# Kernel optimization log

Hardware: AMD Instinct MI355X
Metric: run time of the kernel (lower is better)

Reference implementation:

```python
import jax, jax.numpy as jnp
import numpy as np

B, T, I, R, H = 8, 2048, 128, 1024, 256
LEAKY = 1.0           # leaky_rate
SPECTRAL_RADIUS = 0.9


def setup_inputs() -> dict:
    key = jax.random.key(0)
    ks = jax.random.split(key, 8)
    u = jax.random.normal(ks[0], (B, T, I), dtype=jnp.float32)
    # ESN cell weights (fixed random reservoir)
    w_in = jax.random.normal(ks[1], (R, I), dtype=jnp.float32) * (1.0 / np.sqrt(I))  # input_scaling=1
    w = jax.random.normal(ks[2], (R, R), dtype=jnp.float32) * (SPECTRAL_RADIUS / np.sqrt(R))
    w_bias = jnp.zeros((R,), dtype=jnp.float32)  # bias_scaling=0
    # PCA stand-in: fixed linear projection reservoir -> pca space
    w_pca = jax.random.normal(ks[3], (R, H), dtype=jnp.float32) * (1.0 / np.sqrt(R))
    # gate weights: torch.rand -> uniform [0,1)
    wzp = jax.random.uniform(ks[4], (H, H), dtype=jnp.float32)
    wzh = jax.random.uniform(ks[5], (H, H), dtype=jnp.float32)
    bz = jax.random.uniform(ks[6], (H,), dtype=jnp.float32)
    return {"u": u, "w_in": w_in, "w": w, "w_bias": w_bias,
            "w_pca": w_pca, "wzp": wzp, "wzh": wzh, "bz": bz}


def reference(u, w_in, w, w_bias, w_pca, wzp, wzh, bz):
    Bn = u.shape[0]
    Rd = w.shape[0]
    Hd = bz.shape[0]
    # Precompute input drive for all timesteps: (T, B, R)
    uin = jnp.swapaxes(jnp.einsum('bti,ri->btr', u, w_in) + w_bias, 0, 1)

    # ESN leaky reservoir recurrence: x_t = (1-a)x_{t-1} + a*tanh(W_in u_t + W x_{t-1} + b)
    def res_step(x, u_t):
        x_new = (1.0 - LEAKY) * x + LEAKY * jnp.tanh(u_t + x @ w.T)
        return x_new, x_new

    x0 = jnp.zeros((Bn, Rd), dtype=u.dtype)
    _, res_states = jax.lax.scan(res_step, x0, uin)          # (T, B, R)

    # PCA projection (linear stand-in for fitted IncrementalPCA)
    pca_states = jnp.einsum('tbr,rh->tbh', res_states, w_pca)  # (T, B, H)

    # Gated recurrence: z_t = sigmoid(Wzp p_t + Wzh h_{t-1} + bz); h_t = (1-z)*h + z*p
    def gate_step(h, p):
        z = jax.nn.sigmoid(p @ wzp.T + h @ wzh.T + bz)
        h_new = (1.0 - z) * h + z * p
        return h_new, h_new

    h0 = jnp.zeros((Bn, Hd), dtype=u.dtype)  # per-batch reset_hidden()
    _, hidden_states = jax.lax.scan(gate_step, h0, pca_states)  # (T, B, H)
    return jnp.swapaxes(hidden_states, 0, 1)                    # (B, T, H)
```

## Files before the change

### kernel.cpp

```cpp
#include <hip/hip_runtime.h>

#define TSTEPS 2048
#define NCHAIN 8
#define RDIM 1024
#define IDIM 128
#define HDIM 256
#define NB 16
#define NTHR 512
#define NBLOCKS (NB * NCHAIN)

typedef unsigned long long u64_t;

#define PIN(x) asm volatile("" : "+v"(x))

__device__ __forceinline__ u64_t aload64(const u64_t* p) {
  return __hip_atomic_load(p, __ATOMIC_RELAXED, __HIP_MEMORY_SCOPE_AGENT);
}
__device__ __forceinline__ void astore64(u64_t* p, u64_t v) {
  __hip_atomic_store(p, v, __ATOMIC_RELAXED, __HIP_MEMORY_SCOPE_AGENT);
}
__device__ __forceinline__ u64_t pack(float v, unsigned tag) {
  return ((u64_t)tag << 32) | (u64_t)__float_as_uint(v);
}
__device__ __forceinline__ float val_of(u64_t q) { return __uint_as_float((unsigned)q); }
__device__ __forceinline__ unsigned tag_of(u64_t q) { return (unsigned)(q >> 32); }

__device__ __forceinline__ float wave_sum(float v) {
  v += __shfl_xor(v, 1);
  v += __shfl_xor(v, 2);
  v += __shfl_xor(v, 4);
  v += __shfl_xor(v, 8);
  v += __shfl_xor(v, 16);
  v += __shfl_xor(v, 32);
  return v;
}

__global__ __launch_bounds__(NTHR, 1) void esn_fused(
    const float* __restrict__ u, const float* __restrict__ w_in,
    const float* __restrict__ w, const float* __restrict__ w_bias,
    const float* __restrict__ w_pca, const float* __restrict__ wzp,
    const float* __restrict__ wzh, const float* __restrict__ bz,
    float* __restrict__ out,
    u64_t* __restrict__ x_buf,
    u64_t* __restrict__ p_buf,
    u64_t* __restrict__ h_buf)
{
  const int bid = blockIdx.x;
  const int chain = bid & 7;
  const int sub = bid >> 3;
  const int tid = threadIdx.x;
  const int wave = tid >> 6;
  const int lane = tid & 63;

  __shared__ float lds_x[2][RDIM];
  __shared__ float lds_p[2][HDIM];
  __shared__ float lds_h[2][HDIM];

  const int rrow0 = sub * 64 + wave * 8;
  float4 WA[8][4];
  #pragma unroll
  for (int j = 0; j < 8; ++j)
    #pragma unroll
    for (int i = 0; i < 4; ++i)
      WA[j][i] = *reinterpret_cast<const float4*>(
          w + (size_t)(rrow0 + j) * RDIM + lane * 16 + i * 4);
  float2 Wi[8];
  #pragma unroll
  for (int j = 0; j < 8; ++j)
    Wi[j] = *reinterpret_cast<const float2*>(w_in + (size_t)(rrow0 + j) * IDIM + lane * 2);
  float wb = (lane < 8) ? w_bias[rrow0 + lane] : 0.f;

  const int pcol0 = sub * 16 + wave * 2;
  float Wp[2][16];
  #pragma unroll
  for (int j = 0; j < 2; ++j)
    #pragma unroll
    for (int k = 0; k < 16; ++k)
      Wp[j][k] = w_pca[(size_t)(lane * 16 + k) * HDIM + pcol0 + j];

  const int grow0 = sub * 16 + wave * 2;
  float4 Zp[2], Zh[2];
  #pragma unroll
  for (int j = 0; j < 2; ++j) {
    Zp[j] = *reinterpret_cast<const float4*>(wzp + (size_t)(grow0 + j) * HDIM + lane * 4);
    Zh[j] = *reinterpret_cast<const float4*>(wzh + (size_t)(grow0 + j) * HDIM + lane * 4);
  }
  float bzr = (lane < 2) ? bz[grow0 + lane] : 0.f;

  #pragma unroll
  for (int j = 0; j < 8; ++j)
    #pragma unroll
    for (int i = 0; i < 4; ++i) {
      PIN(WA[j][i].x); PIN(WA[j][i].y); PIN(WA[j][i].z); PIN(WA[j][i].w);
    }
  #pragma unroll
  for (int j = 0; j < 8; ++j) { PIN(Wi[j].x); PIN(Wi[j].y); }
  #pragma unroll
  for (int j = 0; j < 2; ++j)
    #pragma unroll
    for (int k = 0; k < 16; ++k) PIN(Wp[j][k]);
  #pragma unroll
  for (int j = 0; j < 2; ++j) {
    PIN(Zp[j].x); PIN(Zp[j].y); PIN(Zp[j].z); PIN(Zp[j].w);
    PIN(Zh[j].x); PIN(Zh[j].y); PIN(Zh[j].z); PIN(Zh[j].w);
  }
  PIN(wb); PIN(bzr);

  for (int s = 0; s < TSTEPS + 2; ++s) {
    const int cur = s & 1;

    float xc[16];
    const bool xc_valid = (s >= 1 && s <= TSTEPS);
    if (xc_valid) {
      #pragma unroll
      for (int k = 0; k < 16; ++k) xc[k] = lds_x[cur][k * 64 + lane];
    }

    if (s < TSTEPS) {
      float acc[8];
      float2 uu = *reinterpret_cast<const float2*>(
          u + ((size_t)chain * TSTEPS + s) * IDIM + lane * 2);
      #pragma unroll
      for (int j = 0; j < 8; ++j) acc[j] = Wi[j].x * uu.x + Wi[j].y * uu.y;
      if (s > 0) {
        #pragma unroll
        for (int j = 0; j < 8; ++j) {
          float a = acc[j];
          #pragma unroll
          for (int i = 0; i < 4; ++i) {
            a += WA[j][i].x * xc[i * 4 + 0];
            a += WA[j][i].y * xc[i * 4 + 1];
            a += WA[j][i].z * xc[i * 4 + 2];
            a += WA[j][i].w * xc[i * 4 + 3];
          }
          acc[j] = a;
        }
      }
      #pragma unroll
      for (int j = 0; j < 8; ++j) acc[j] = wave_sum(acc[j]);
      float v = acc[0];
      #pragma unroll
      for (int j = 1; j < 8; ++j) v = (lane == j) ? acc[j] : v;
      if (lane < 8)
        astore64(x_buf + (((s & 1) * NCHAIN) + chain) * RDIM + rrow0 + lane,
                 pack(tanhf(v + wb), (unsigned)(s + 1)));
    }

    if (xc_valid) {
      const int t = s - 1;
      float a0 = 0.f, a1 = 0.f;
      #pragma unroll
      for (int k = 0; k < 16; ++k) { a0 += Wp[0][k] * xc[k]; a1 += Wp[1][k] * xc[k]; }
      a0 = wave_sum(a0);
      a1 = wave_sum(a1);
      float v = (lane == 1) ? a1 : a0;
      if (lane < 2)
        astore64(p_buf + (((t & 3) * NCHAIN) + chain) * HDIM + pcol0 + lane,
                 pack(v, (unsigned)(t + 1)));
    }

    if (s >= 2) {
      const int t = s - 2;
      float pc[4], hc[4];
      #pragma unroll
      for (int k = 0; k < 4; ++k) pc[k] = lds_p[cur][k * 64 + lane];
      if (t > 0) {
        #pragma unroll
        for (int k = 0; k < 4; ++k) hc[k] = lds_h[cur][k * 64 + lane];
      } else {
        hc[0] = hc[1] = hc[2] = hc[3] = 0.f;
      }
      float a0 = Zp[0].x * pc[0] + Zp[0].y * pc[1] + Zp[0].z * pc[2] + Zp[0].w * pc[3]
               + Zh[0].x * hc[0] + Zh[0].y * hc[1] + Zh[0].z * hc[2] + Zh[0].w * hc[3];
      float a1 = Zp[1].x * pc[0] + Zp[1].y * pc[1] + Zp[1].z * pc[2] + Zp[1].w * pc[3]
               + Zh[1].x * hc[0] + Zh[1].y * hc[1] + Zh[1].z * hc[2] + Zh[1].w * hc[3];
      a0 = wave_sum(a0);
      a1 = wave_sum(a1);
      float v = (lane == 1) ? a1 : a0;
      if (lane < 2) {
        const int row = grow0 + lane;
        float z = 1.f / (1.f + expf(-(v + bzr)));
        float pt = lds_p[cur][(row & 3) * 64 + (row >> 2)];
        float hp = (t > 0) ? lds_h[cur][(row & 3) * 64 + (row >> 2)] : 0.f;
        float hnew = hp + z * (pt - hp);
        astore64(h_buf + (((t & 3) * NCHAIN) + chain) * HDIM + row,
                 pack(hnew, (unsigned)(t + 1)));
        out[((size_t)chain * TSTEPS + t) * HDIM + row] = hnew;
      }
    }

    const int nxt = (s + 1) & 1;
    if (wave == 0) {
      if (s <= TSTEPS - 1) {
        const u64_t* xp =
            x_buf + (((s & 1) * NCHAIN) + chain) * RDIM + lane * 16;
        const unsigned want = (unsigned)(s + 1);
        u64_t q[16];
        unsigned it = 0;
        for (;;) {
          bool ok = true;
          #pragma unroll
          for (int k = 0; k < 16; ++k) q[k] = aload64(xp + k);
          #pragma unroll
          for (int k = 0; k < 16; ++k) ok = ok & (tag_of(q[k]) == want);
          if (ok) break;
          __builtin_amdgcn_s_sleep(1);
          if (++it > (1u << 17)) break;
        }
        #pragma unroll
        for (int k = 0; k < 16; ++k) lds_x[nxt][k * 64 + lane] = val_of(q[k]);
      }
    } else if (wave == 1) {
      const bool needp = (s >= 1 && s <= TSTEPS);
      const bool needh = (s >= 2 && s <= TSTEPS);
      if (needp) {
        const u64_t* pvp =
            p_buf + ((((s - 1) & 3) * NCHAIN) + chain) * HDIM + lane * 4;
        const u64_t* hvp =
            h_buf + ((((s - 2) & 3) * NCHAIN) + chain) * HDIM + lane * 4;
        const unsigned wantp = (unsigned)s;
        const unsigned wanth = (unsigned)(s - 1);
        u64_t qp[4], qh[4];
        unsigned it = 0;
        for (;;) {
          bool ok = true;
          #pragma unroll
          for (int k = 0; k < 4; ++k) qp[k] = aload64(pvp + k);
          if (needh) {
            #pragma unroll
            for (int k = 0; k < 4; ++k) qh[k] = aload64(hvp + k);
          }
          #pragma unroll
          for (int k = 0; k < 4; ++k) ok = ok & (tag_of(qp[k]) == wantp);
          if (needh) {
            #pragma unroll
            for (int k = 0; k < 4; ++k) ok = ok & (tag_of(qh[k]) == wanth);
          }
          if (ok) break;
          __builtin_amdgcn_s_sleep(1);
          if (++it > (1u << 17)) break;
        }
        #pragma unroll
        for (int k = 0; k < 4; ++k) lds_p[nxt][k * 64 + lane] = val_of(qp[k]);
        if (needh) {
          #pragma unroll
          for (int k = 0; k < 4; ++k) lds_h[nxt][k * 64 + lane] = val_of(qh[k]);
        }
      }
    }
    __syncthreads();
  }
}

extern "C" void kernel_launch(void* const* d_in, const int* in_sizes, int n_in,
                              void* d_out, int out_size, void* d_ws, size_t ws_size,
                              hipStream_t stream) {
  const float* ptrs[8] = {nullptr};
  const int want[8] = {TSTEPS * NCHAIN * IDIM, RDIM * IDIM, RDIM * RDIM, RDIM,
                       RDIM * HDIM, HDIM * HDIM, HDIM * HDIM, HDIM};
  if (n_in == 8) {
    int used[8] = {0};
    for (int k = 0; k < 8; ++k)
      for (int i = 0; i < n_in; ++i)
        if (!used[i] && in_sizes[i] == want[k]) {
          ptrs[k] = (const float*)d_in[i]; used[i] = 1; break;
        }
  }
  bool ok = true;
  for (int k = 0; k < 8; ++k) ok = ok && (ptrs[k] != nullptr);
  if (!ok)
    for (int k = 0; k < 8; ++k) ptrs[k] = (const float*)d_in[k];

  float* out = (float*)d_out;

  u64_t* x_buf = (u64_t*)d_ws;
  u64_t* p_buf = x_buf + 2 * NCHAIN * RDIM;
  u64_t* h_buf = p_buf + 4 * NCHAIN * HDIM;
  size_t need_u64 = (size_t)(2 * NCHAIN * RDIM + 2 * 4 * NCHAIN * HDIM);
  if (ws_size < need_u64 * 8) return;

  esn_fused<<<dim3(NBLOCKS), dim3(NTHR), 0, stream>>>(
      ptrs[0], ptrs[1], ptrs[2], ptrs[3], ptrs[4], ptrs[5], ptrs[6], ptrs[7],
      out, x_buf, p_buf, h_buf);
}
```

Before: 11.78 ms.

## Interleave two batch chains per block to hide cross-block sync latency

Each block now handles two batch chains in alternating slots instead of one, so the grid shrinks from 128 to 64 blocks. While one chain's cross-block exchange of reservoir state is in flight, the block computes the other chain's step. This is meant to hide the global-memory polling latency of the per-timestep dependency. In exchange each block does twice as many slots serially, and the weights held in registers are shared across both chains.

```diff
diff --git a/kernel.cpp b/kernel.cpp
--- a/kernel.cpp
+++ b/kernel.cpp
@@ -5,9 +5,11 @@
 #define RDIM 1024
 #define IDIM 128
 #define HDIM 256
+#define KFOLD 2
+#define NSETS (NCHAIN / KFOLD)
 #define NB 16
 #define NTHR 512
-#define NBLOCKS (NB * NCHAIN)
+#define NBLOCKS (NB * NSETS)
 
 typedef unsigned long long u64_t;
 
@@ -46,8 +48,8 @@
     u64_t* __restrict__ h_buf)
 {
   const int bid = blockIdx.x;
-  const int chain = bid & 7;
-  const int sub = bid >> 3;
+  const int sub = bid & (NB - 1);
+  const int set = bid >> 4;
   const int tid = threadIdx.x;
   const int wave = tid >> 6;
   const int lane = tid & 63;
@@ -106,8 +108,13 @@
   }
   PIN(wb); PIN(bzr);
 
-  for (int s = 0; s < TSTEPS + 2; ++s) {
-    const int cur = s & 1;
+  const int NSLOT = KFOLD * (TSTEPS + 2);
+  for (int slot = 0; slot < NSLOT; ++slot) {
+    const int ci = slot & 1;
+    const int chain = set * KFOLD + ci;
+    const int s = slot >> 1;
+    const int cur = slot & 1;
+    const int nxt = (slot + 1) & 1;
 
     float xc[16];
     const bool xc_valid = (s >= 1 && s <= TSTEPS);
@@ -189,62 +196,66 @@
       }
     }
 
-    const int nxt = (s + 1) & 1;
-    if (wave == 0) {
-      if (s <= TSTEPS - 1) {
-        const u64_t* xp =
-            x_buf + (((s & 1) * NCHAIN) + chain) * RDIM + lane * 16;
-        const unsigned want = (unsigned)(s + 1);
-        u64_t q[16];
-        unsigned it = 0;
-        for (;;) {
-          bool ok = true;
+    {
+      const int c1 = set * KFOLD + ((slot + 1) & 1);
+      const int s1 = (slot + 1) >> 1;
+      if (wave == 0) {
+        const bool needx = (s1 >= 1 && s1 <= TSTEPS);
+        if (needx) {
+          const u64_t* xp =
+              x_buf + ((((s1 - 1) & 1) * NCHAIN) + c1) * RDIM + lane * 16;
+          const unsigned want = (unsigned)s1;
+          u64_t q[16];
+          unsigned it = 0;
+          for (;;) {
+            bool ok = true;
+            #pragma unroll
+            for (int k = 0; k < 16; ++k) q[k] = aload64(xp + k);
+            #pragma unroll
+            for (int k = 0; k < 16; ++k) ok = ok & (tag_of(q[k]) == want);
+            if (ok) break;
+            __builtin_amdgcn_s_sleep(1);
+            if (++it > (1u << 17)) break;
+          }
           #pragma unroll
-          for (int k = 0; k < 16; ++k) q[k] = aload64(xp + k);
+          for (int k = 0; k < 16; ++k) lds_x[nxt][k * 64 + lane] = val_of(q[k]);
+        }
+      } else if (wave == 1) {
+        const bool needp = (s1 >= 2 && s1 <= TSTEPS + 1);
+        const bool needh = (s1 >= 3 && s1 <= TSTEPS + 1);
+        if (needp) {
+          const u64_t* pvp =
+              p_buf + ((((s1 - 2) & 3) * NCHAIN) + c1) * HDIM + lane * 4;
+          const u64_t* hvp =
+              h_buf + ((((s1 - 3) & 3) * NCHAIN) + c1) * HDIM + lane * 4;
+          const unsigned wantp = (unsigned)(s1 - 1);
+          const unsigned wanth = (unsigned)(s1 - 2);
+          u64_t qp[4], qh[4];
+          unsigned it = 0;
+          for (;;) {
+            bool ok = true;
+            #pragma unroll
+            for (int k = 0; k < 4; ++k) qp[k] = aload64(pvp + k);
+            if (needh) {
+              #pragma unroll
+              for (int k = 0; k < 4; ++k) qh[k] = aload64(hvp + k);
+            }
+            #pragma unroll
+            for (int k = 0; k < 4; ++k) ok = ok & (tag_of(qp[k]) == wantp);
+            if (needh) {
+              #pragma unroll
+              for (int k = 0; k < 4; ++k) ok = ok & (tag_of(qh[k]) == wanth);
+            }
+            if (ok) break;
+            __builtin_amdgcn_s_sleep(1);
+            if (++it > (1u << 17)) break;
+          }
           #pragma unroll
-          for (int k = 0; k < 16; ++k) ok = ok & (tag_of(q[k]) == want);
-          if (ok) break;
-          __builtin_amdgcn_s_sleep(1);
-          if (++it > (1u << 17)) break;
-        }
-        #pragma unroll
-        for (int k = 0; k < 16; ++k) lds_x[nxt][k * 64 + lane] = val_of(q[k]);
-      }
-    } else if (wave == 1) {
-      const bool needp = (s >= 1 && s <= TSTEPS);
-      const bool needh = (s >= 2 && s <= TSTEPS);
-      if (needp) {
-        const u64_t* pvp =
-            p_buf + ((((s - 1) & 3) * NCHAIN) + chain) * HDIM + lane * 4;
-        const u64_t* hvp =
-            h_buf + ((((s - 2) & 3) * NCHAIN) + chain) * HDIM + lane * 4;
-        const unsigned wantp = (unsigned)s;
-        const unsigned wanth = (unsigned)(s - 1);
-        u64_t qp[4], qh[4];
-        unsigned it = 0;
-        for (;;) {
-          bool ok = true;
-          #pragma unroll
-          for (int k = 0; k < 4; ++k) qp[k] = aload64(pvp + k);
+          for (int k = 0; k < 4; ++k) lds_p[nxt][k * 64 + lane] = val_of(qp[k]);
           if (needh) {
             #pragma unroll
-            for (int k = 0; k < 4; ++k) qh[k] = aload64(hvp + k);
-          }
-          #pragma unroll
-          for (int k = 0; k < 4; ++k) ok = ok & (tag_of(qp[k]) == wantp);
-          if (needh) {
-            #pragma unroll
-            for (int k = 0; k < 4; ++k) ok = ok & (tag_of(qh[k]) == wanth);
-          }
-          if (ok) break;
-          __builtin_amdgcn_s_sleep(1);
-          if (++it > (1u << 17)) break;
-        }
-        #pragma unroll
-        for (int k = 0; k < 4; ++k) lds_p[nxt][k * 64 + lane] = val_of(qp[k]);
-        if (needh) {
-          #pragma unroll
-          for (int k = 0; k < 4; ++k) lds_h[nxt][k * 64 + lane] = val_of(qh[k]);
+            for (int k = 0; k < 4; ++k) lds_h[nxt][k * 64 + lane] = val_of(qh[k]);
+          }
         }
       }
     }
```

Result: slower. 21.77 ms (+84.7%).
